# Performance work log

Hardware: AMD Instinct MI355X
Metric: run time of the kernel (lower is better)

## Reference

```python
import jax, jax.numpy as jnp
import numpy as np
jax.config.update("jax_enable_x64", True)

WINDOW_SHAPE = (16, 16, 8)
SPARSE_SHAPE = (512, 512, 64)
GROUP_SIZE = 128
BATCH_COUNTS = np.array([500000, 480123, 510007, 495870], dtype=np.int64)  # not multiples of 128 -> padding path active


def setup_inputs() -> dict:
    key = jax.random.key(0)
    kx, ky, kz = jax.random.split(key, 3)
    N = int(BATCH_COUNTS.sum())
    bids = jnp.asarray(np.repeat(np.arange(len(BATCH_COUNTS), dtype=np.int64), BATCH_COUNTS))
    x = jax.random.randint(kx, (N,), 0, SPARSE_SHAPE[0], dtype=jnp.int64)
    y = jax.random.randint(ky, (N,), 0, SPARSE_SHAPE[1], dtype=jnp.int64)
    z = jax.random.randint(kz, (N,), 0, SPARSE_SHAPE[2], dtype=jnp.int64)
    coords = jnp.stack([bids, x, y, z], axis=1)  # [N,4] int64: (batch, x, y, z)
    return {"coords": coords, "batch_size": 4}


def _hash_keys(coords, shifted):
    n, m, l = SPARSE_SHAPE
    n2o, m2o, l2o = WINDOW_SHAPE
    n1 = int(np.ceil(n / n2o) + 1)
    m1 = int(np.ceil(m / m2o) + 1)
    l1 = int(np.ceil(l / l2o) + 1)
    if shifted:
        x = coords[:, 1] + n2o // 2
        y = coords[:, 2] + m2o // 2
        z = coords[:, 3] + l2o // 2
    else:
        x, y, z = coords[:, 1], coords[:, 2], coords[:, 3]
    x1, y1, z1 = x // n2o, y // m2o, z // l2o
    x2, y2, z2 = x % n2o, y % m2o, z % l2o
    # original code triples both window and grid-of-window extents before hashing
    n2, m2, l2 = 3 * n2o, 3 * m2o, 3 * l2o
    n1, m1, l1 = 3 * n1, 3 * m1, 3 * l1
    sx = 1 - 2 * (x1 & 1)  # (-1)**x1
    sy = 1 - 2 * (y1 & 1)
    sz = 1 - 2 * (z1 & 1)
    s2x = 1 - 2 * (x2 & 1)
    s2y = 1 - 2 * (y2 & 1)
    s2z = 1 - 2 * (z2 & 1)
    boff = coords[:, 0] * (n * m * l * 10)
    vx = (n1 * y1 + n1 * m1 * z1 + sy * x1) * (n2 * m2 * l2) + sy * (m2 * x2 + n2 * m2 * z2 + s2x * y2) + boff
    vy = (m1 * z1 + m1 * l1 * x1 + sz * y1) * (m2 * l2 * n2) + sz * (l2 * y2 + m2 * l2 * x2 + s2y * z2) + boff
    vz = (l1 * x1 + l1 * n1 * y1 + sx * z1) * (l2 * n2 * m2) + sx * (n2 * z2 + l2 * n2 * y2 + s2z * x2) + boff
    return vx, vy, vz


def reference(coords, batch_size):
    G = GROUP_SIZE
    coords = coords.astype(jnp.int64)
    bids = coords[:, 0]
    N = coords.shape[0]
    num_per_batch = jax.ops.segment_sum(jnp.ones((N,), jnp.int64), bids, num_segments=batch_size)
    bs = jnp.concatenate([jnp.zeros((1,), jnp.int64), jnp.cumsum(num_per_batch)])
    num_per_batch_p = ((num_per_batch + G - 1) // G) * G
    bsp = jnp.concatenate([jnp.zeros((1,), jnp.int64), jnp.cumsum(num_per_batch_p)])
    Np = int(bsp[-1])  # concrete (not under jit); padded total length

    # win2flat[j] = j + (bsp[b] - bs[b]) for b = batch of element j (coords assumed batch-sorted)
    win2flat = jnp.arange(N, dtype=jnp.int64) + (bsp[:-1] - bs[:-1])[bids]

    # flat2win: identity within each padded batch, with the padded tail replicated
    # from one group earlier, then shifted back to flat indexing.
    p = jnp.arange(Np, dtype=jnp.int64)
    b = jnp.searchsorted(bsp, p, side="right") - 1  # batch of each padded slot
    r = num_per_batch % G
    pad_tail = (r[b] != 0) & (p >= bsp[b + 1] - G + r[b])
    flat2win = p - G * pad_tail.astype(jnp.int64) - (bsp[b] - bs[b])

    outs = [flat2win, win2flat]
    for shifted in (False, True):
        vx, vy, vz = _hash_keys(coords, shifted)
        outs.append(jnp.argsort(vx))
        outs.append(jnp.argsort(vy))
        outs.append(jnp.argsort(vz))
    # (flat2win, win2flat, x, y, z, x_shift, y_shift, z_shift)
    return tuple(outs)
```

## Files before the change

### kernel.cpp

```cpp
#include <hip/hip_runtime.h>
#include <type_traits>

typedef unsigned long long u64;
typedef unsigned int u32;

#define BLOCK     256
#define WAVES     4
#define TILE      4096
#define SUBT      1024
#define CHUNKS    16
#define KSHIFT    21
#define KBIAS     (1LL << 21)
#define KMASK     ((1u << 21) - 1)
#define GRP       128


__device__ __forceinline__ void hash3(long long x, long long y, long long z,
                                      long long boff, long long* v) {
  long long x1 = x >> 4, y1 = y >> 4, z1 = z >> 3;
  long long x2 = x & 15, y2 = y & 15, z2 = z & 7;
  long long sx  = 1 - 2*(x1 & 1), sy  = 1 - 2*(y1 & 1), sz  = 1 - 2*(z1 & 1);
  long long s2x = 1 - 2*(x2 & 1), s2y = 1 - 2*(y2 & 1), s2z = 1 - 2*(z2 & 1);
  v[0] = (99*y1 + 9801*z1 + sy*x1)*55296 + sy*(48*x2 + 2304*z2 + s2x*y2) + boff;
  v[1] = (99*z1 + 2673*x1 + sz*y1)*55296 + sz*(24*y2 + 1152*x2 + s2y*z2) + boff;
  v[2] = (27*x1 + 2673*y1 + sx*z1)*55296 + sx*(48*z2 + 1152*y2 + s2z*x2) + boff;
}

__global__ void count_k(const int* __restrict__ coords, unsigned* __restrict__ counts, int N) {
  __shared__ unsigned c[8];
  if (threadIdx.x < 8) c[threadIdx.x] = 0;
  __syncthreads();
  for (int i = blockIdx.x*blockDim.x + threadIdx.x; i < N; i += gridDim.x*blockDim.x)
    atomicAdd(&c[coords[4*i] & 7], 1u);
  __syncthreads();
  if (threadIdx.x < 8) atomicAdd(&counts[threadIdx.x], c[threadIdx.x]);
}

__global__ void prefix_k(const unsigned* __restrict__ counts, long long* __restrict__ meta,
                         const int* __restrict__ bsz) {
  int NB = *bsz; if (NB > 8) NB = 8;
  long long run_bs = 0, run_bsp = 0;
  meta[0] = 0;
  for (int b = 0; b < NB; b++) {
    long long c  = (long long)counts[b];
    long long cp = (c + GRP - 1) / GRP * GRP;
    long long r  = c % GRP;
    meta[9 + b]  = run_bsp - run_bs;
    meta[17 + b] = r ? (run_bsp + cp - GRP + r) : 0x7fffffffffffffffLL;
    run_bs += c; run_bsp += cp;
    meta[b + 1] = run_bsp;
  }
  meta[25] = run_bsp;
  meta[26] = NB;
}

__global__ void flat2win_k(const long long* __restrict__ meta, int* __restrict__ dout) {
  long long p = (long long)blockIdx.x * blockDim.x + threadIdx.x;
  long long Np = meta[25];
  if (p >= Np) return;
  int NB = (int)meta[26];
  int b = 0;
  while (b < NB - 1 && meta[b + 1] <= p) b++;
  long long pad = (p >= meta[17 + b]) ? 1 : 0;
  dout[p] = (int)(p - GRP * pad - meta[9 + b]);
}

__global__ void __launch_bounds__(BLOCK) keygen_k(const int* __restrict__ coords,
                                                  u64* __restrict__ keys,
                                                  u32* __restrict__ hist,
                                                  const long long* __restrict__ meta,
                                                  int* __restrict__ dout,
                                                  int N, int B, int g0, int g, int doAux) {
  __shared__ u32 cnt[6 * 256];
  int b = blockIdx.x, tid = threadIdx.x;
  int nb = g * 256;
  for (int j = tid; j < nb; j += BLOCK) cnt[j] = 0;
  __syncthreads();
  long long Np = meta[25];
  for (int t = 0; t < CHUNKS; t++) {
    int i = b * TILE + t * BLOCK + tid;
    if (i < N) {
      int4 c4 = ((const int4*)coords)[i];
      long long boff = (long long)c4.x * 167772160LL;
      long long v[6];
      hash3(c4.y,     c4.z,     c4.w,     boff, v);
      hash3(c4.y + 8, c4.z + 8, c4.w + 4, boff, v + 3);
      #pragma unroll
      for (int s = 0; s < 6; s++) {
        if (s >= g0 && s < g0 + g) {
          u64 kb = (u64)(v[s] + KBIAS);
          keys[(size_t)(s - g0) * N + i] = (kb << KSHIFT) | (unsigned)i;
          atomicAdd(&cnt[(s - g0) * 256 + ((unsigned)kb & 255)], 1u);
        }
      }
      if (doAux) dout[Np + i] = (int)(i + meta[9 + c4.x]);
    }
  }
  __syncthreads();
  for (int j = tid; j < nb; j += BLOCK) {
    int s = j >> 8, d = j & 255;
    hist[((size_t)s * 256 + d) * B + b] = cnt[j];
  }
}

template<typename KT, int RADIXN, int SHIFT>
__global__ void __launch_bounds__(BLOCK) hist_k(const KT* __restrict__ src,
                                                u32* __restrict__ hist, int N, int B) {
  __shared__ u32 cnt[RADIXN];
  int s = blockIdx.y, b = blockIdx.x, tid = threadIdx.x;
  for (int j = tid; j < RADIXN; j += BLOCK) cnt[j] = 0;
  __syncthreads();
  const KT* in = src + (size_t)s * N;
  #pragma unroll 4
  for (int t = 0; t < CHUNKS; t++) {
    int i = b * TILE + t * BLOCK + tid;
    if (i < N) {
      unsigned d = (unsigned)(in[i] >> SHIFT) & (RADIXN - 1);
      atomicAdd(&cnt[d], 1u);
    }
  }
  __syncthreads();
  for (int j = tid; j < RADIXN; j += BLOCK) hist[((size_t)s * RADIXN + j) * B + b] = cnt[j];
}

template<int RADIXN>
__global__ void __launch_bounds__(BLOCK) scanA_k(u32* __restrict__ hist,
                                                 u32* __restrict__ dbase, int B) {
  int s = blockIdx.y;
  int d = blockIdx.x * WAVES + (threadIdx.x >> 6);
  int lane = threadIdx.x & 63;
  u32* row = hist + ((size_t)s * RADIXN + d) * B;
  u32 run = 0;
  for (int b0 = 0; b0 < B; b0 += 64) {
    int b = b0 + lane;
    u32 v = (b < B) ? row[b] : 0;
    u32 x = v;
    #pragma unroll
    for (int off = 1; off < 64; off <<= 1) { u32 u = __shfl_up(x, off); if (lane >= off) x += u; }
    if (b < B) row[b] = run + x - v;
    run += __shfl(x, 63);
  }
  if (lane == 0) dbase[(size_t)s * 512 + d] = run;
}

template<int RADIXN>
__global__ void __launch_bounds__(64) scanB_k(u32* __restrict__ dbase) {
  int s = blockIdx.x, tid = threadIdx.x;
  u32 run = 0;
  #pragma unroll
  for (int c = 0; c < RADIXN / 64; c++) {
    int dd = c * 64 + tid;
    u32 v = dbase[(size_t)s * 512 + dd], x = v;
    for (int off = 1; off < 64; off <<= 1) { u32 u = __shfl_up(x, off); if (tid >= off) x += u; }
    dbase[(size_t)s * 512 + dd] = run + x - v;
    run += __shfl(x, 63);
  }
}

template<int RB, int SHIFT, int MODE>
__global__ void __launch_bounds__(BLOCK) scatter_k(const void* __restrict__ srcv,
                                                   void* __restrict__ dstv,
                                                   const u32* __restrict__ hist,
                                                   const u32* __restrict__ dbase,
                                                   int N, int B,
                                                   int* __restrict__ dout,
                                                   const long long* __restrict__ meta, int g0) {
  constexpr int RADIXN = 1 << RB;
  constexpr int DPT = (RADIXN + BLOCK - 1) / BLOCK;
  using KT = typename std::conditional<MODE == 2, u32, u64>::type;
  using ST = typename std::conditional<MODE == 0, u64, u32>::type;
  __shared__ ST items[TILE];
  __shared__ unsigned short dig[MODE == 1 ? TILE : 64];
  __shared__ unsigned short cnt[WAVES][RADIXN];
  __shared__ int exf[RADIXN];
  int s, b;
  {
    int nwg = B * (int)gridDim.y;
    int lin = (int)blockIdx.y * B + (int)blockIdx.x;
    int qc = nwg >> 3, rc = nwg & 7;
    int xcd = lin & 7, pos = lin >> 3;
    int swz = (xcd < rc ? xcd * (qc + 1) : rc * (qc + 1) + (xcd - rc) * qc) + pos;
    s = swz / B; b = swz - s * B;
  }
  int tid = threadIdx.x;
  int wave = tid >> 6, lane = tid & 63;
  for (int j = tid; j < WAVES * RADIXN; j += BLOCK) ((unsigned short*)cnt)[j] = 0;
  __syncthreads();

  const KT* in = (const KT*)srcv + (size_t)s * N;
  int subbase = b * TILE + wave * SUBT;
  bool full = (subbase + SUBT <= N);
  KT k[CHUNKS]; u32 pd[CHUNKS];
  if (full) {
    #pragma unroll
    for (int t = 0; t < CHUNKS; t++) k[t] = in[subbase + t * 64 + lane];
    #pragma unroll
    for (int t = 0; t < CHUNKS; t++) {
      unsigned d = (unsigned)(k[t] >> SHIFT) & (RADIXN - 1);
      u64 m = ~0ull;
      #pragma unroll
      for (int bit = 0; bit < RB; bit++) {
        u64 bal = __ballot((d >> bit) & 1);
        m &= ((d >> bit) & 1) ? bal : ~bal;
      }
      unsigned rank = __builtin_amdgcn_mbcnt_hi((u32)(m >> 32),
                        __builtin_amdgcn_mbcnt_lo((u32)m, 0u));
      unsigned pbase = cnt[wave][d];
      pd[t] = d | ((pbase + rank) << RB);
      if (rank == 0) cnt[wave][d] = (unsigned short)(pbase + (unsigned)__popcll(m));
    }
  } else {
    #pragma unroll
    for (int t = 0; t < CHUNKS; t++) k[t] = in[min(subbase + t * 64 + lane, N - 1)];
    #pragma unroll
    for (int t = 0; t < CHUNKS; t++) {
      int i = subbase + t * 64 + lane;
      bool valid = i < N;
      unsigned d = (unsigned)(k[t] >> SHIFT) & (RADIXN - 1);
      u64 m = __ballot(valid);
      #pragma unroll
      for (int bit = 0; bit < RB; bit++) {
        u64 bal = __ballot(valid && ((d >> bit) & 1));
        m &= ((d >> bit) & 1) ? bal : ~bal;
      }
      unsigned rank = __builtin_amdgcn_mbcnt_hi((u32)(m >> 32),
                        __builtin_amdgcn_mbcnt_lo((u32)m, 0u));
      unsigned pbase = cnt[wave][d];
      pd[t] = d | ((pbase + rank) << RB);
      if (valid && rank == 0) cnt[wave][d] = (unsigned short)(pbase + (unsigned)__popcll(m));
    }
  }
  __syncthreads();

  u32 sc[DPT][3];
  #pragma unroll
  for (int q = 0; q < DPT; q++) {
    int d = q * BLOCK + tid;
    u32 a0 = cnt[0][d], a1 = cnt[1][d], a2 = cnt[2][d], a3 = cnt[3][d];
    sc[q][0] = a0; sc[q][1] = a1; sc[q][2] = a2;
    exf[d] = (int)(a0 + a1 + a2 + a3);
  }
  __syncthreads();
  if (tid < 64) {
    u32 run = 0;
    #pragma unroll
    for (int c = 0; c < (RADIXN + 63) / 64; c++) {
      int dd = c * 64 + tid;
      u32 v = (u32)exf[dd], x = v;
      for (int off = 1; off < 64; off <<= 1) { u32 u = __shfl_up(x, off); if (tid >= off) x += u; }
      exf[dd] = (int)(run + x - v);
      run += __shfl(x, 63);
    }
  }
  __syncthreads();
  const u32* brow = dbase + (size_t)s * 512;
  #pragma unroll
  for (int q = 0; q < DPT; q++) {
    int d = q * BLOCK + tid;
    int e = exf[d];
    u32 gb = hist[((size_t)s * RADIXN + d) * B + b] + brow[d];
    cnt[0][d] = (unsigned short)e;
    cnt[1][d] = (unsigned short)(e + sc[q][0]);
    cnt[2][d] = (unsigned short)(e + sc[q][0] + sc[q][1]);
    cnt[3][d] = (unsigned short)(e + sc[q][0] + sc[q][1] + sc[q][2]);
    exf[d] = (int)gb - e;
  }
  __syncthreads();

  #pragma unroll
  for (int t = 0; t < CHUNKS; t++) {
    int i = subbase + t * 64 + lane;
    if (i < N) {
      unsigned d = pd[t] & (RADIXN - 1);
      unsigned lr = pd[t] >> RB;
      unsigned pos = (unsigned)cnt[wave][d] + lr;
      if constexpr (MODE == 1) {
        items[pos] = (u32)(((k[t] >> 46) << 21) | ((u32)k[t] & KMASK));
        dig[pos] = (unsigned short)d;
      } else {
        items[pos] = (ST)k[t];
      }
    }
  }
  __syncthreads();

  int validCount = N - b * TILE; if (validCount > TILE) validCount = TILE;
  long long obase = 0;
  if (MODE == 2) obase = meta[25] + (long long)N * (1 + g0 + s);
  u64* out64 = (u64*)dstv + (size_t)s * N;
  u32* out32 = (u32*)dstv + (size_t)s * N;
  #pragma unroll 4
  for (int t = 0; t < CHUNKS; t++) {
    int j = t * BLOCK + tid;
    if (j < validCount) {
      ST kk = items[j];
      if constexpr (MODE == 0) {
        unsigned d = (unsigned)(kk >> SHIFT) & (RADIXN - 1);
        out64[exf[d] + j] = kk;
      } else if constexpr (MODE == 1) {
        unsigned d = dig[j];
        out32[exf[d] + j] = kk;
      } else {
        unsigned d = (unsigned)(kk >> SHIFT) & (RADIXN - 1);
        dout[obase + exf[d] + j] = (int)(kk & KMASK);
      }
    }
  }
}

extern "C" void kernel_launch(void* const* d_in, const int* in_sizes, int n_in,
                              void* d_out, int out_size, void* d_ws, size_t ws_size,
                              hipStream_t stream) {
  const int* coords = (const int*)d_in[0];
  const int* bsz    = (const int*)d_in[1];
  int N = in_sizes[0] / 4;
  int* dout = (int*)d_out;
  char* ws = (char*)d_ws;
  int B = (N + TILE - 1) / TILE;

  auto align256 = [](size_t x) { return (x + 255) & ~(size_t)255; };

  int g = 1;
  size_t offHist = 512, offBase = 0, offA = 0, offB = 0;
  const int cands[4] = {6, 3, 2, 1};
  for (int ci = 0; ci < 4; ci++) {
    int cg = cands[ci];
    size_t oBs = offHist + (size_t)cg * B * 512 * 4;
    size_t oA = align256(oBs + (size_t)cg * 512 * 4);
    size_t oB = oA + (size_t)cg * N * 8;
    size_t need = oB + (size_t)cg * N * 8;
    if (need <= ws_size || cg == 1) {
      g = cg; offBase = oBs; offA = oA; offB = oB;
      if (need <= ws_size) break;
    }
  }

  unsigned*  counts = (unsigned*)ws;
  long long* meta   = (long long*)(ws + 64);
  u32*       hist   = (u32*)(ws + offHist);
  u32*       dbase  = (u32*)(ws + offBase);
  u64*       keysA  = (u64*)(ws + offA);
  u64*       keysB  = (u64*)(ws + offB);

  hipMemsetAsync(ws, 0, 512, stream);
  count_k<<<1024, 256, 0, stream>>>(coords, counts, N);
  prefix_k<<<1, 1, 0, stream>>>(counts, meta, bsz);
  flat2win_k<<<(N + 8 * GRP + 255) / 256, 256, 0, stream>>>(meta, dout);

  for (int g0 = 0; g0 < 6; g0 += g) {
    keygen_k<<<B, BLOCK, 0, stream>>>(coords, keysA, hist, meta, dout, N, B, g0, g, g0 == 0);
    scanA_k<256><<<dim3(256 / WAVES, g), BLOCK, 0, stream>>>(hist, dbase, B);
    scanB_k<256><<<g, 64, 0, stream>>>(dbase);
    scatter_k<8, 21, 0><<<dim3(B, g), BLOCK, 0, stream>>>(keysA, keysB, hist, dbase, N, B,
                                                          dout, meta, g0);
    hist_k<u64, 256, 29><<<dim3(B, g), BLOCK, 0, stream>>>(keysB, hist, N, B);
    scanA_k<256><<<dim3(256 / WAVES, g), BLOCK, 0, stream>>>(hist, dbase, B);
    scanB_k<256><<<g, 64, 0, stream>>>(dbase);
    scatter_k<8, 29, 0><<<dim3(B, g), BLOCK, 0, stream>>>(keysB, keysA, hist, dbase, N, B,
                                                          dout, meta, g0);
    hist_k<u64, 512, 37><<<dim3(B, g), BLOCK, 0, stream>>>(keysA, hist, N, B);
    scanA_k<512><<<dim3(512 / WAVES, g), BLOCK, 0, stream>>>(hist, dbase, B);
    scanB_k<512><<<g, 64, 0, stream>>>(dbase);
    scatter_k<9, 37, 1><<<dim3(B, g), BLOCK, 0, stream>>>(keysA, keysB, hist, dbase, N, B,
                                                          dout, meta, g0);
    hist_k<u32, 256, 21><<<dim3(B, g), BLOCK, 0, stream>>>((const u32*)keysB, hist, N, B);
    scanA_k<256><<<dim3(256 / WAVES, g), BLOCK, 0, stream>>>(hist, dbase, B);
    scanB_k<256><<<g, 64, 0, stream>>>(dbase);
    scatter_k<8, 21, 2><<<dim3(B, g), BLOCK, 0, stream>>>(keysB, keysA, hist, dbase, N, B,
                                                          dout, meta, g0);
  }
}
```

Measured before the change: 394.6 us.

## Fold digit-base scan into scatter, fuse flat2win into keygen, narrow hash to int32

Removes the separate scanB kernel launches by having a second wave in each scatter block redo the exclusive scan of per-digit totals into shared memory. It also folds the flat2win kernel into the first keygen pass and computes the hash intermediates in 32-bit ints before widening. The goal is fewer kernel launches and serial dependencies per radix pass, plus cheaper integer math. In exchange every scatter block repeats the digit-total scan redundantly, and the first keygen pass takes on the flat2win writes.

```diff
diff --git a/kernel.cpp b/kernel.cpp
--- a/kernel.cpp
+++ b/kernel.cpp
@@ -15,15 +15,18 @@
 #define GRP       128
 
 
-__device__ __forceinline__ void hash3(long long x, long long y, long long z,
+__device__ __forceinline__ void hash3(int x, int y, int z,
                                       long long boff, long long* v) {
-  long long x1 = x >> 4, y1 = y >> 4, z1 = z >> 3;
-  long long x2 = x & 15, y2 = y & 15, z2 = z & 7;
-  long long sx  = 1 - 2*(x1 & 1), sy  = 1 - 2*(y1 & 1), sz  = 1 - 2*(z1 & 1);
-  long long s2x = 1 - 2*(x2 & 1), s2y = 1 - 2*(y2 & 1), s2z = 1 - 2*(z2 & 1);
-  v[0] = (99*y1 + 9801*z1 + sy*x1)*55296 + sy*(48*x2 + 2304*z2 + s2x*y2) + boff;
-  v[1] = (99*z1 + 2673*x1 + sz*y1)*55296 + sz*(24*y2 + 1152*x2 + s2y*z2) + boff;
-  v[2] = (27*x1 + 2673*y1 + sx*z1)*55296 + sx*(48*z2 + 1152*y2 + s2z*x2) + boff;
+  int x1 = x >> 4, y1 = y >> 4, z1 = z >> 3;
+  int x2 = x & 15, y2 = y & 15, z2 = z & 7;
+  int sx  = 1 - 2*(x1 & 1), sy  = 1 - 2*(y1 & 1), sz  = 1 - 2*(z1 & 1);
+  int s2x = 1 - 2*(x2 & 1), s2y = 1 - 2*(y2 & 1), s2z = 1 - 2*(z2 & 1);
+  v[0] = (long long)(99*y1 + 9801*z1 + sy*x1) * 55296
+         + (sy*(48*x2 + 2304*z2 + s2x*y2)) + boff;
+  v[1] = (long long)(99*z1 + 2673*x1 + sz*y1) * 55296
+         + (sz*(24*y2 + 1152*x2 + s2y*z2)) + boff;
+  v[2] = (long long)(27*x1 + 2673*y1 + sx*z1) * 55296
+         + (sx*(48*z2 + 1152*y2 + s2z*x2)) + boff;
 }
 
 __global__ void count_k(const int* __restrict__ coords, unsigned* __restrict__ counts, int N) {
@@ -52,17 +55,6 @@
   }
   meta[25] = run_bsp;
   meta[26] = NB;
-}
-
-__global__ void flat2win_k(const long long* __restrict__ meta, int* __restrict__ dout) {
-  long long p = (long long)blockIdx.x * blockDim.x + threadIdx.x;
-  long long Np = meta[25];
-  if (p >= Np) return;
-  int NB = (int)meta[26];
-  int b = 0;
-  while (b < NB - 1 && meta[b + 1] <= p) b++;
-  long long pad = (p >= meta[17 + b]) ? 1 : 0;
-  dout[p] = (int)(p - GRP * pad - meta[9 + b]);
 }
 
 __global__ void __launch_bounds__(BLOCK) keygen_k(const int* __restrict__ coords,
@@ -96,6 +88,27 @@
       if (doAux) dout[Np + i] = (int)(i + meta[9 + c4.x]);
     }
   }
+  if (doAux) {
+    int NB = (int)meta[26];
+    for (int t = 0; t < CHUNKS; t++) {
+      long long p = (long long)b * TILE + t * BLOCK + tid;
+      if (p < Np) {
+        int bb = 0;
+        while (bb < NB - 1 && meta[bb + 1] <= p) bb++;
+        long long pad = (p >= meta[17 + bb]) ? 1 : 0;
+        dout[p] = (int)(p - GRP * pad - meta[9 + bb]);
+      }
+    }
+    if (b == B - 1) {
+      int NB2 = (int)meta[26];
+      for (long long p = (long long)B * TILE + tid; p < Np; p += BLOCK) {
+        int bb = 0;
+        while (bb < NB2 - 1 && meta[bb + 1] <= p) bb++;
+        long long pad = (p >= meta[17 + bb]) ? 1 : 0;
+        dout[p] = (int)(p - GRP * pad - meta[9 + bb]);
+      }
+    }
+  }
   __syncthreads();
   for (int j = tid; j < nb; j += BLOCK) {
     int s = j >> 8, d = j & 255;
@@ -141,20 +154,6 @@
     run += __shfl(x, 63);
   }
   if (lane == 0) dbase[(size_t)s * 512 + d] = run;
-}
-
-template<int RADIXN>
-__global__ void __launch_bounds__(64) scanB_k(u32* __restrict__ dbase) {
-  int s = blockIdx.x, tid = threadIdx.x;
-  u32 run = 0;
-  #pragma unroll
-  for (int c = 0; c < RADIXN / 64; c++) {
-    int dd = c * 64 + tid;
-    u32 v = dbase[(size_t)s * 512 + dd], x = v;
-    for (int off = 1; off < 64; off <<= 1) { u32 u = __shfl_up(x, off); if (tid >= off) x += u; }
-    dbase[(size_t)s * 512 + dd] = run + x - v;
-    run += __shfl(x, 63);
-  }
 }
 
 template<int RB, int SHIFT, int MODE>
@@ -173,6 +172,7 @@
   __shared__ unsigned short dig[MODE == 1 ? TILE : 64];
   __shared__ unsigned short cnt[WAVES][RADIXN];
   __shared__ int exf[RADIXN];
+  __shared__ u32 gbl[RADIXN];
   int s, b;
   {
     int nwg = B * (int)gridDim.y;
@@ -241,24 +241,34 @@
     exf[d] = (int)(a0 + a1 + a2 + a3);
   }
   __syncthreads();
-  if (tid < 64) {
+  if (wave == 0) {
     u32 run = 0;
     #pragma unroll
     for (int c = 0; c < (RADIXN + 63) / 64; c++) {
-      int dd = c * 64 + tid;
+      int dd = c * 64 + lane;
       u32 v = (u32)exf[dd], x = v;
-      for (int off = 1; off < 64; off <<= 1) { u32 u = __shfl_up(x, off); if (tid >= off) x += u; }
+      for (int off = 1; off < 64; off <<= 1) { u32 u = __shfl_up(x, off); if (lane >= off) x += u; }
       exf[dd] = (int)(run + x - v);
       run += __shfl(x, 63);
     }
-  }
-  __syncthreads();
-  const u32* brow = dbase + (size_t)s * 512;
+  } else if (wave == 1) {
+    const u32* brow = dbase + (size_t)s * 512;
+    u32 run = 0;
+    #pragma unroll
+    for (int c = 0; c < (RADIXN + 63) / 64; c++) {
+      int dd = c * 64 + lane;
+      u32 v = brow[dd], x = v;
+      for (int off = 1; off < 64; off <<= 1) { u32 u = __shfl_up(x, off); if (lane >= off) x += u; }
+      gbl[dd] = run + x - v;
+      run += __shfl(x, 63);
+    }
+  }
+  __syncthreads();
   #pragma unroll
   for (int q = 0; q < DPT; q++) {
     int d = q * BLOCK + tid;
     int e = exf[d];
-    u32 gb = hist[((size_t)s * RADIXN + d) * B + b] + brow[d];
+    u32 gb = hist[((size_t)s * RADIXN + d) * B + b] + gbl[d];
     cnt[0][d] = (unsigned short)e;
     cnt[1][d] = (unsigned short)(e + sc[q][0]);
     cnt[2][d] = (unsigned short)(e + sc[q][0] + sc[q][1]);
@@ -345,27 +355,22 @@
   hipMemsetAsync(ws, 0, 512, stream);
   count_k<<<1024, 256, 0, stream>>>(coords, counts, N);
   prefix_k<<<1, 1, 0, stream>>>(counts, meta, bsz);
-  flat2win_k<<<(N + 8 * GRP + 255) / 256, 256, 0, stream>>>(meta, dout);
 
   for (int g0 = 0; g0 < 6; g0 += g) {
     keygen_k<<<B, BLOCK, 0, stream>>>(coords, keysA, hist, meta, dout, N, B, g0, g, g0 == 0);
     scanA_k<256><<<dim3(256 / WAVES, g), BLOCK, 0, stream>>>(hist, dbase, B);
-    scanB_k<256><<<g, 64, 0, stream>>>(dbase);
     scatter_k<8, 21, 0><<<dim3(B, g), BLOCK, 0, stream>>>(keysA, keysB, hist, dbase, N, B,
                                                           dout, meta, g0);
     hist_k<u64, 256, 29><<<dim3(B, g), BLOCK, 0, stream>>>(keysB, hist, N, B);
     scanA_k<256><<<dim3(256 / WAVES, g), BLOCK, 0, stream>>>(hist, dbase, B);
-    scanB_k<256><<<g, 64, 0, stream>>>(dbase);
     scatter_k<8, 29, 0><<<dim3(B, g), BLOCK, 0, stream>>>(keysB, keysA, hist, dbase, N, B,
                                                           dout, meta, g0);
     hist_k<u64, 512, 37><<<dim3(B, g), BLOCK, 0, stream>>>(keysA, hist, N, B);
     scanA_k<512><<<dim3(512 / WAVES, g), BLOCK, 0, stream>>>(hist, dbase, B);
-    scanB_k<512><<<g, 64, 0, stream>>>(dbase);
     scatter_k<9, 37, 1><<<dim3(B, g), BLOCK, 0, stream>>>(keysA, keysB, hist, dbase, N, B,
                                                           dout, meta, g0);
     hist_k<u32, 256, 21><<<dim3(B, g), BLOCK, 0, stream>>>((const u32*)keysB, hist, N, B);
     scanA_k<256><<<dim3(256 / WAVES, g), BLOCK, 0, stream>>>(hist, dbase, B);
-    scanB_k<256><<<g, 64, 0, stream>>>(dbase);
     scatter_k<8, 21, 2><<<dim3(B, g), BLOCK, 0, stream>>>(keysB, keysA, hist, dbase, N, B,
                                                           dout, meta, g0);
   }
```

Measured after the change: 395.7 us. No clear change (+0.3%).
